# Kernel tuning notes

Hardware: AMD Instinct MI355X
Metric: run time of the kernel (lower is better)

Reference implementation:

```python
import jax, jax.numpy as jnp
import numpy as np

B, N, E = 256, 128, 262144
LABEL_DIM, MAX_DEGREE, RW_DIM = 29, 16, 16
F = 128
NUM_LABELS = LABEL_DIM + MAX_DEGREE + RW_DIM  # 61
SK_ITER, SK_TAU = 6, 1.0


def _edges(k):
    k1, k2, k3 = jax.random.split(k, 3)
    g = jax.random.randint(k1, (E,), 0, B)
    src = g * N + jax.random.randint(k2, (E,), 0, N)
    dst = g * N + jax.random.randint(k3, (E,), 0, N)
    return src, dst


def setup_inputs():
    key = jax.random.key(0)
    ks = jax.random.split(key, 20)
    ntot = B * N
    s = 0.05
    nrm = lambda k, shp: jax.random.normal(k, shp, dtype=jnp.float32) * s
    src1, dst1 = _edges(ks[3])
    src2, dst2 = _edges(ks[7])
    return {
        'x1': jax.random.uniform(ks[0], (ntot, LABEL_DIM), dtype=jnp.float32),
        'cent1': jax.random.randint(ks[1], (ntot,), 0, MAX_DEGREE),
        'rw1': jax.random.uniform(ks[2], (ntot, RW_DIM), dtype=jnp.float32),
        'src1': src1, 'dst1': dst1,
        'x2': jax.random.uniform(ks[4], (ntot, LABEL_DIM), dtype=jnp.float32),
        'cent2': jax.random.randint(ks[5], (ntot,), 0, MAX_DEGREE),
        'rw2': jax.random.uniform(ks[6], (ntot, RW_DIM), dtype=jnp.float32),
        'src2': src2, 'dst2': dst2,
        'degree_emb': nrm(ks[8], (MAX_DEGREE, MAX_DEGREE)),
        'init_W': nrm(ks[9], (NUM_LABELS, F)), 'init_b': jnp.zeros((F,), jnp.float32),
        'W1': nrm(ks[10], (F, F)), 'b1': jnp.zeros((F,), jnp.float32),
        'W2': nrm(ks[11], (F, F)), 'b2': jnp.zeros((F,), jnp.float32),
        'W3': nrm(ks[12], (F, F)), 'b3': jnp.zeros((F,), jnp.float32),
        'A_aff': nrm(ks[13], (F, F)) + jnp.eye(F, dtype=jnp.float32),
        'sc_W1': nrm(ks[14], (8 * F, 64)), 'sc_b1': jnp.zeros((64,), jnp.float32),
        'sc_W2': nrm(ks[15], (64, 1)), 'sc_b2': jnp.zeros((1,), jnp.float32),
        'topk': 8,
    }


def gcn_conv(x, W, b, src, dst):
    # GCNConv: x' = D^{-1/2} (A + I) D^{-1/2} x W + b
    n = x.shape[0]
    h = x @ W
    loops = jnp.arange(n)
    s = jnp.concatenate([src, loops])
    d = jnp.concatenate([dst, loops])
    deg = jax.ops.segment_sum(jnp.ones_like(d, dtype=h.dtype), d, n)
    dinv = jax.lax.rsqrt(jnp.maximum(deg, 1.0))
    w = dinv[s] * dinv[d]
    return jax.ops.segment_sum(h[s] * w[:, None], d, n) + b


def conv_pass(feat, src, dst, W1, b1, W2, b2, W3, b3):
    f1 = gcn_conv(feat, W1, b1, src, dst)
    f2 = gcn_conv(jax.nn.relu(f1), W2, b2, src, dst)
    f3 = gcn_conv(jax.nn.relu(f2), W3, b3, src, dst)
    return f1, f2, f3


def affinity(xa, xb, A):
    Xa = xa.reshape(B, N, -1)
    Xb = xb.reshape(B, N, -1)
    return jnp.einsum('bif,fg,bjg->bij', Xa, A, Xb)


def soft_topk(scores, ks_tgt, n_iter, tau):
    # Entropic-OT soft top-k (Xie et al.) over flattened affinity entries vs 2 anchors,
    # normalized by SK_ITER log-domain Sinkhorn iterations.
    b, n, m = scores.shape
    L = n * m
    x = scores.reshape(b, L)
    a_lo = x.min(axis=1, keepdims=True) - 1.0
    a_hi = x.max(axis=1, keepdims=True) + 1.0
    anchors = jnp.concatenate([a_lo, a_hi], axis=1)      # [b, 2]
    logK = -jnp.abs(x[:, :, None] - anchors[:, None, :]) / tau  # [b, L, 2]
    log_mu = jnp.full((b, L), -jnp.log(float(L)), dtype=x.dtype)
    k = ks_tgt[:, None]
    nu = jnp.concatenate([(L - k) / L, k / L], axis=1)   # [b, 2]
    log_nu = jnp.log(nu)

    def body(carry, _):
        f, g = carry
        f = log_mu - jax.nn.logsumexp(logK + g[:, None, :], axis=2)
        g = log_nu - jax.nn.logsumexp(logK + f[:, :, None], axis=1)
        return (f, g), None

    init = (jnp.zeros((b, L), x.dtype), jnp.zeros((b, 2), x.dtype))
    (f, g), _ = jax.lax.scan(body, init, None, length=n_iter)
    gamma = jnp.exp(logK + f[:, :, None] + g[:, None, :])
    prob = (gamma[:, :, 1] * L).reshape(b, n, m)
    return gamma, prob


def reference(x1, cent1, rw1, src1, dst1, x2, cent2, rw2, src2, dst2,
              degree_emb, init_W, init_b, W1, b1, W2, b2, W3, b3, A_aff,
              sc_W1, sc_b1, sc_W2, sc_b2, topk):
    feat1 = jax.nn.relu(jnp.concatenate([x1, degree_emb[cent1], rw1], axis=1) @ init_W + init_b)
    feat2 = jax.nn.relu(jnp.concatenate([x2, degree_emb[cent2], rw2], axis=1) @ init_W + init_b)
    f11, f12, f13 = conv_pass(feat1, src1, dst1, W1, b1, W2, b2, W3, b3)
    f21, f22, f23 = conv_pass(feat2, src2, dst2, W1, b1, W2, b2, W3, b3)

    gt_ks = jnp.full((B,), topk / 2.0, dtype=feat1.dtype)
    _, sim1 = soft_topk(affinity(feat1, feat2, A_aff), gt_ks, SK_ITER, SK_TAU)
    _, sim2 = soft_topk(affinity(f13, f23, A_aff), gt_ks, SK_ITER, SK_TAU)

    gf1 = jnp.concatenate([feat1, f11, f12, f13], axis=1).reshape(B, N, -1).sum(axis=1)   # global_add_pool
    gf2 = jnp.concatenate([feat2, f21, f22, f23], axis=1).reshape(B, N, -1).max(axis=1)   # global_max_pool
    scores = jnp.concatenate([gf1, gf2], axis=1)  # [B, 8F]
    h = jax.nn.relu(scores @ sc_W1 + sc_b1)
    ged = jax.nn.sigmoid((h @ sc_W2 + sc_b2).reshape(-1))
    return ged, sim1, sim2
```

## Files before the change

kernel.cpp:

```cpp
#include <hip/hip_runtime.h>
#include <math.h>

#define BATCH 256
#define NNODE 128
#define NT    32768
#define FDIM  128
#define NEDGE 262144
#define LBL   29
#define MAXDEG 16
#define RWD   16
#define NTF   (NT * FDIM)

__global__ void k_deg2(const int* __restrict__ dst1, const int* __restrict__ dst2,
                       int* __restrict__ d1, int* __restrict__ d2) {
  int e = blockIdx.x * 256 + threadIdx.x;
  if (e < NEDGE) atomicAdd(&d1[dst1[e]], 1);
  else if (e < 2 * NEDGE) atomicAdd(&d2[dst2[e - NEDGE]], 1);
}
__global__ __launch_bounds__(1024) void k_scan2(const int* __restrict__ degi1,
                                                int* __restrict__ ofs1, int* __restrict__ cur1,
                                                float* __restrict__ dinv1,
                                                const int* __restrict__ degi2,
                                                int* __restrict__ ofs2, int* __restrict__ cur2,
                                                float* __restrict__ dinv2) {
  const int* degi = blockIdx.x ? degi2 : degi1;
  int* ofs   = blockIdx.x ? ofs2  : ofs1;
  int* cur   = blockIdx.x ? cur2  : cur1;
  float* dnv = blockIdx.x ? dinv2 : dinv1;
  __shared__ int part[1024];
  int t = threadIdx.x;
  int base = t * 32;
  int loc[32]; int sum = 0;
#pragma unroll
  for (int u = 0; u < 32; ++u) {
    int dg = degi[base + u];
    loc[u] = sum; sum += dg;
    dnv[base + u] = rsqrtf((float)(dg + 1));
  }
  part[t] = sum;
  __syncthreads();
  for (int off = 1; off < 1024; off <<= 1) {
    int v = (t >= off) ? part[t - off] : 0;
    __syncthreads();
    part[t] += v;
    __syncthreads();
  }
  int excl = (t == 0) ? 0 : part[t - 1];
#pragma unroll
  for (int u = 0; u < 32; ++u) {
    int o = excl + loc[u];
    ofs[base + u] = o; cur[base + u] = o;
  }
}
__global__ void k_fill2(const int* __restrict__ src1, const int* __restrict__ dst1,
                        int* __restrict__ cur1, int* __restrict__ csr1,
                        const int* __restrict__ src2, const int* __restrict__ dst2,
                        int* __restrict__ cur2, int* __restrict__ csr2) {
  int e = blockIdx.x * 256 + threadIdx.x;
  if (e < NEDGE) {
    int pos = atomicAdd(&cur1[dst1[e]], 1);
    csr1[pos] = src1[e];
  } else if (e < 2 * NEDGE) {
    e -= NEDGE;
    int pos = atomicAdd(&cur2[dst2[e]], 1);
    csr2[pos] = src2[e];
  }
}

__global__ __launch_bounds__(256, 2) void k_chain(
    const float* __restrict__ x1, const int* __restrict__ cent1, const float* __restrict__ rw1,
    const float* __restrict__ x2, const int* __restrict__ cent2, const float* __restrict__ rw2,
    const float* __restrict__ demb,
    const float* __restrict__ initW, const float* __restrict__ initb,
    const float* __restrict__ W1, const float* __restrict__ b1,
    const float* __restrict__ W2, const float* __restrict__ b2,
    const float* __restrict__ W3, const float* __restrict__ b3,
    const int* __restrict__ ofs1, const int* __restrict__ end1, const int* __restrict__ csr1,
    const int* __restrict__ ofs2, const int* __restrict__ end2, const int* __restrict__ csr2,
    const float* __restrict__ dinv1, const float* __restrict__ dinv2,
    float* __restrict__ feat1G, float* __restrict__ feat2G,
    float* __restrict__ f13G, float* __restrict__ f23G,
    float* __restrict__ gfs) {
  __shared__ float X[128 * 132];
  __shared__ float WcB[16 * 132];
  __shared__ float dvL[128];
  __shared__ float bL[128];
  __shared__ int   oL[128], enL[128];

  const int t = threadIdx.x;
  const int side = blockIdx.x >> 8;
  const int g = blockIdx.x & 255;
  const int nb = g * NNODE;

  const float* xg    = side ? x2 : x1;
  const int*   centg = side ? cent2 : cent1;
  const float* rwg   = side ? rw2 : rw1;
  const int*   ofsg  = side ? ofs2 : ofs1;
  const int*   endg  = side ? end2 : end1;
  const int*   csrg  = side ? csr2 : csr1;
  const float* dinvg = side ? dinv2 : dinv1;
  float* featG = side ? feat2G : feat1G;
  float* f3G   = side ? f23G : f13G;

  const int e_base = ofsg[nb];
  if (t < 128) {
    dvL[t] = dinvg[nb + t];
    oL[t]  = ofsg[nb + t] - e_base;
    enL[t] = endg[nb + t] - e_base;
  }
  {
    int d = t >> 1, sub = t & 1;
    int node = nb + d;
    int ct = centg[node];
    const float* xr = xg + (size_t)node * LBL;
    const float* er = demb + ct * MAXDEG;
    const float* rr = rwg + (size_t)node * RWD;
    for (int c = sub * 34; c < sub * 34 + 34; ++c) {
      float v = 0.f;
      if (c < LBL) v = xr[c];
      else if (c < LBL + MAXDEG) v = er[c - LBL];
      else if (c < 61) v = rr[c - 45];
      X[d * 68 + c] = v;
    }
  }
  __syncthreads();

  const int rg = t >> 3;
  const int jq = (t & 7) * 4;

  {
    float acc[4][16] = {};
    for (int kc = 0; kc < 64; kc += 16) {
      __syncthreads();
#pragma unroll
      for (int u = 0; u < 2; ++u) {
        int ll = t + 256 * u;
        int row = ll >> 5, c4 = (ll & 31) * 4;
        int gk = kc + row;
        float4 w = (gk < 61) ? *reinterpret_cast<const float4*>(&initW[(size_t)gk * FDIM + c4])
                             : make_float4(0.f, 0.f, 0.f, 0.f);
        *reinterpret_cast<float4*>(&WcB[row * 132 + c4]) = w;
      }
      if (kc == 0 && t < 128) bL[t] = initb[t];
      __syncthreads();
      for (int kk = 0; kk < 16; kk += 4) {
        float av[4][4];
#pragma unroll
        for (int r = 0; r < 4; ++r) {
          float4 tmp = *reinterpret_cast<const float4*>(&X[(rg + 32 * r) * 68 + kc + kk]);
          av[r][0] = tmp.x; av[r][1] = tmp.y; av[r][2] = tmp.z; av[r][3] = tmp.w;
        }
#pragma unroll
        for (int c = 0; c < 4; ++c) {
          float4 w0 = *reinterpret_cast<const float4*>(&WcB[(kk + c) * 132 + jq]);
          float4 w1 = *reinterpret_cast<const float4*>(&WcB[(kk + c) * 132 + 32 + jq]);
          float4 w2 = *reinterpret_cast<const float4*>(&WcB[(kk + c) * 132 + 64 + jq]);
          float4 w3 = *reinterpret_cast<const float4*>(&WcB[(kk + c) * 132 + 96 + jq]);
#pragma unroll
          for (int r = 0; r < 4; ++r) {
            float a = av[r][c];
            acc[r][0]  += a * w0.x; acc[r][1]  += a * w0.y; acc[r][2]  += a * w0.z; acc[r][3]  += a * w0.w;
            acc[r][4]  += a * w1.x; acc[r][5]  += a * w1.y; acc[r][6]  += a * w1.z; acc[r][7]  += a * w1.w;
            acc[r][8]  += a * w2.x; acc[r][9]  += a * w2.y; acc[r][10] += a * w2.z; acc[r][11] += a * w2.w;
            acc[r][12] += a * w3.x; acc[r][13] += a * w3.y; acc[r][14] += a * w3.z; acc[r][15] += a * w3.w;
          }
        }
      }
    }
    __syncthreads();
#pragma unroll
    for (int r = 0; r < 4; ++r) {
      int row = rg + 32 * r;
#pragma unroll
      for (int q = 0; q < 4; ++q) {
        int col = q * 32 + jq;
        float4 bl = *reinterpret_cast<const float4*>(&bL[col]);
        float4 o = make_float4(fmaxf(acc[r][q * 4 + 0] + bl.x, 0.f),
                               fmaxf(acc[r][q * 4 + 1] + bl.y, 0.f),
                               fmaxf(acc[r][q * 4 + 2] + bl.z, 0.f),
                               fmaxf(acc[r][q * 4 + 3] + bl.w, 0.f));
        *reinterpret_cast<float4*>(&X[row * 132 + col]) = o;
        *reinterpret_cast<float4*>(&featG[(size_t)(nb + row) * FDIM + col]) = o;
      }
    }
    __syncthreads();
  }

#define POOL_LAYER(layer)                                                            \
  {                                                                                  \
    int j4 = (t & 31) * 4, qq = t >> 5;                                              \
    float4 pv = side ? make_float4(-INFINITY, -INFINITY, -INFINITY, -INFINITY)       \
                     : make_float4(0.f, 0.f, 0.f, 0.f);                              \
    for (int r = 0; r < 16; ++r) {                                                   \
      float4 fv = *reinterpret_cast<const float4*>(&X[(qq * 16 + r) * 132 + j4]);    \
      if (side) { pv.x = fmaxf(pv.x, fv.x); pv.y = fmaxf(pv.y, fv.y);                \
                  pv.z = fmaxf(pv.z, fv.z); pv.w = fmaxf(pv.w, fv.w); }              \
      else      { pv.x += fv.x; pv.y += fv.y; pv.z += fv.z; pv.w += fv.w; }          \
    }                                                                                \
    *reinterpret_cast<float4*>(&WcB[qq * 128 + j4]) = pv;                            \
    __syncthreads();                                                                 \
    if (t < 128) {                                                                   \
      float v = side ? -INFINITY : 0.f;                                              \
      for (int q2 = 0; q2 < 8; ++q2) {                                               \
        float w2 = WcB[q2 * 128 + t];                                                \
        v = side ? fmaxf(v, w2) : (v + w2);                                          \
      }                                                                              \
      gfs[g * 1024 + side * 512 + (layer) * 128 + t] = v;                            \
    }                                                                                \
  }

  POOL_LAYER(0)

  for (int l = 0; l < 3; ++l) {
    const float* Wg = (l == 0) ? W1 : (l == 1) ? W2 : W3;
    const float* bg = (l == 0) ? b1 : (l == 1) ? b2 : b3;
    float acc[4][16] = {};
    for (int kc = 0; kc < 128; kc += 16) {
      __syncthreads();
#pragma unroll
      for (int u = 0; u < 2; ++u) {
        int ll = t + 256 * u;
        int row = ll >> 5, c4 = (ll & 31) * 4;
        *reinterpret_cast<float4*>(&WcB[row * 132 + c4]) =
            *reinterpret_cast<const float4*>(&Wg[(size_t)(kc + row) * FDIM + c4]);
      }
      if (kc == 0 && t < 128) bL[t] = bg[t];
      __syncthreads();
      for (int kk = 0; kk < 16; kk += 4) {
        float av[4][4];
#pragma unroll
        for (int r = 0; r < 4; ++r) {
          float4 tmp = *reinterpret_cast<const float4*>(&X[(rg + 32 * r) * 132 + kc + kk]);
          if (l > 0) {
            tmp.x = fmaxf(tmp.x, 0.f); tmp.y = fmaxf(tmp.y, 0.f);
            tmp.z = fmaxf(tmp.z, 0.f); tmp.w = fmaxf(tmp.w, 0.f);
          }
          av[r][0] = tmp.x; av[r][1] = tmp.y; av[r][2] = tmp.z; av[r][3] = tmp.w;
        }
#pragma unroll
        for (int c = 0; c < 4; ++c) {
          float4 w0 = *reinterpret_cast<const float4*>(&WcB[(kk + c) * 132 + jq]);
          float4 w1 = *reinterpret_cast<const float4*>(&WcB[(kk + c) * 132 + 32 + jq]);
          float4 w2 = *reinterpret_cast<const float4*>(&WcB[(kk + c) * 132 + 64 + jq]);
          float4 w3 = *reinterpret_cast<const float4*>(&WcB[(kk + c) * 132 + 96 + jq]);
#pragma unroll
          for (int r = 0; r < 4; ++r) {
            float a = av[r][c];
            acc[r][0]  += a * w0.x; acc[r][1]  += a * w0.y; acc[r][2]  += a * w0.z; acc[r][3]  += a * w0.w;
            acc[r][4]  += a * w1.x; acc[r][5]  += a * w1.y; acc[r][6]  += a * w1.z; acc[r][7]  += a * w1.w;
            acc[r][8]  += a * w2.x; acc[r][9]  += a * w2.y; acc[r][10] += a * w2.z; acc[r][11] += a * w2.w;
            acc[r][12] += a * w3.x; acc[r][13] += a * w3.y; acc[r][14] += a * w3.z; acc[r][15] += a * w3.w;
          }
        }
      }
    }
    __syncthreads();
#pragma unroll
    for (int r = 0; r < 4; ++r) {
      int row = rg + 32 * r;
#pragma unroll
      for (int q = 0; q < 4; ++q) {
        int col = q * 32 + jq;
        *reinterpret_cast<float4*>(&X[row * 132 + col]) =
            make_float4(acc[r][q * 4 + 0], acc[r][q * 4 + 1],
                        acc[r][q * 4 + 2], acc[r][q * 4 + 3]);
      }
    }
    __syncthreads();

    {
      int d = t >> 1, fc = (t & 1) * 64;
      float dd = dvL[d];
      float4 a[16];
#pragma unroll
      for (int u = 0; u < 16; ++u) {
        float4 hv = *reinterpret_cast<const float4*>(&X[d * 132 + fc + u * 4]);
        a[u] = make_float4(dd * hv.x, dd * hv.y, dd * hv.z, dd * hv.w);
      }
      int o0 = oL[d], o1 = enL[d];
      int sj = (o0 < o1) ? (csrg[e_base + o0] - nb) : 0;
      for (int j = o0; j < o1; ++j) {
        int sn = (j + 1 < o1) ? (csrg[e_base + j + 1] - nb) : 0;
        float w = dvL[sj];
#pragma unroll
        for (int u = 0; u < 16; ++u) {
          float4 hv = *reinterpret_cast<const float4*>(&X[sj * 132 + fc + u * 4]);
          a[u].x += w * hv.x; a[u].y += w * hv.y; a[u].z += w * hv.z; a[u].w += w * hv.w;
        }
        sj = sn;
      }
      __syncthreads();
#pragma unroll
      for (int u = 0; u < 16; ++u) {
        float4 bl = *reinterpret_cast<const float4*>(&bL[fc + u * 4]);
        float4 o = make_float4(bl.x + dd * a[u].x, bl.y + dd * a[u].y,
                               bl.z + dd * a[u].z, bl.w + dd * a[u].w);
        *reinterpret_cast<float4*>(&X[d * 132 + fc + u * 4]) = o;
        if (l == 2)
          *reinterpret_cast<float4*>(&f3G[(size_t)(nb + d) * FDIM + fc + u * 4]) = o;
      }
    }
    __syncthreads();

    POOL_LAYER(l + 1)
  }
#undef POOL_LAYER
}

__global__ __launch_bounds__(1024) void k_sim(const float* __restrict__ F1s1,
                                              const float* __restrict__ F2s1,
                                              const float* __restrict__ F1s2,
                                              const float* __restrict__ F2s2,
                                              const float* __restrict__ Aaff,
                                              const int* __restrict__ topk,
                                              float* __restrict__ S1,
                                              float* __restrict__ S2) {
  __shared__ float X1[128 * 132];
  __shared__ float X2[128 * 132];
  __shared__ float WcB[16 * 132];
  __shared__ float rA[16], rB[16], bc[2];

  const int t = threadIdx.x;
  const int half = blockIdx.x >> 8;
  const int b = blockIdx.x & 255;
  const float* F1b = (half ? F1s2 : F1s1) + (size_t)b * NNODE * FDIM;
  const float* F2b = (half ? F2s2 : F2s1) + (size_t)b * NNODE * FDIM;
  float* Sout = (half ? S2 : S1) + (size_t)b * NNODE * NNODE;

#pragma unroll
  for (int p = 0; p < 4; ++p) {
    int fi = t + 1024 * p;
    int row = fi >> 5, c4 = (fi & 31) * 4;
    *reinterpret_cast<float4*>(&X1[row * 132 + c4]) =
        *reinterpret_cast<const float4*>(&F1b[(size_t)row * FDIM + c4]);
    *reinterpret_cast<float4*>(&X2[row * 132 + c4]) =
        *reinterpret_cast<const float4*>(&F2b[(size_t)row * FDIM + c4]);
  }

  const int rg = t >> 3;
  const int jq = (t & 7) * 4;

  float acc[16];
#pragma unroll
  for (int u = 0; u < 16; ++u) acc[u] = 0.f;

  for (int kc = 0; kc < 128; kc += 16) {
    __syncthreads();
    if (t < 512) {
      int row = t >> 5, c4 = (t & 31) * 4;
      *reinterpret_cast<float4*>(&WcB[row * 132 + c4]) =
          *reinterpret_cast<const float4*>(&Aaff[(size_t)(kc + row) * FDIM + c4]);
    }
    __syncthreads();
    for (int kk = 0; kk < 16; kk += 4) {
      float4 a4 = *reinterpret_cast<const float4*>(&X1[rg * 132 + kc + kk]);
      float av[4] = {a4.x, a4.y, a4.z, a4.w};
#pragma unroll
      for (int c = 0; c < 4; ++c) {
        float4 w0 = *reinterpret_cast<const float4*>(&WcB[(kk + c) * 132 + jq]);
        float4 w1 = *reinterpret_cast<const float4*>(&WcB[(kk + c) * 132 + 32 + jq]);
        float4 w2 = *reinterpret_cast<const float4*>(&WcB[(kk + c) * 132 + 64 + jq]);
        float4 w3 = *reinterpret_cast<const float4*>(&WcB[(kk + c) * 132 + 96 + jq]);
        float a = av[c];
        acc[0]  += a * w0.x; acc[1]  += a * w0.y; acc[2]  += a * w0.z; acc[3]  += a * w0.w;
        acc[4]  += a * w1.x; acc[5]  += a * w1.y; acc[6]  += a * w1.z; acc[7]  += a * w1.w;
        acc[8]  += a * w2.x; acc[9]  += a * w2.y; acc[10] += a * w2.z; acc[11] += a * w2.w;
        acc[12] += a * w3.x; acc[13] += a * w3.y; acc[14] += a * w3.z; acc[15] += a * w3.w;
      }
    }
  }
  __syncthreads();
#pragma unroll
  for (int q = 0; q < 4; ++q)
    *reinterpret_cast<float4*>(&X1[rg * 132 + 32 * q + jq]) =
        make_float4(acc[q * 4 + 0], acc[q * 4 + 1], acc[q * 4 + 2], acc[q * 4 + 3]);

#pragma unroll
  for (int u = 0; u < 16; ++u) acc[u] = 0.f;

  for (int kc = 0; kc < 128; kc += 16) {
    __syncthreads();
#pragma unroll
    for (int p = 0; p < 2; ++p) {
      int id = t + 1024 * p;
      int kkr = id >> 7, c = id & 127;
      WcB[kkr * 132 + c] = X2[c * 132 + kc + kkr];
    }
    __syncthreads();
    for (int kk = 0; kk < 16; kk += 4) {
      float4 a4 = *reinterpret_cast<const float4*>(&X1[rg * 132 + kc + kk]);
      float av[4] = {a4.x, a4.y, a4.z, a4.w};
#pragma unroll
      for (int c = 0; c < 4; ++c) {
        float4 w0 = *reinterpret_cast<const float4*>(&WcB[(kk + c) * 132 + jq]);
        float4 w1 = *reinterpret_cast<const float4*>(&WcB[(kk + c) * 132 + 32 + jq]);
        float4 w2 = *reinterpret_cast<const float4*>(&WcB[(kk + c) * 132 + 64 + jq]);
        float4 w3 = *reinterpret_cast<const float4*>(&WcB[(kk + c) * 132 + 96 + jq]);
        float a = av[c];
        acc[0]  += a * w0.x; acc[1]  += a * w0.y; acc[2]  += a * w0.z; acc[3]  += a * w0.w;
        acc[4]  += a * w1.x; acc[5]  += a * w1.y; acc[6]  += a * w1.z; acc[7]  += a * w1.w;
        acc[8]  += a * w2.x; acc[9]  += a * w2.y; acc[10] += a * w2.z; acc[11] += a * w2.w;
        acc[12] += a * w3.x; acc[13] += a * w3.y; acc[14] += a * w3.z; acc[15] += a * w3.w;
      }
    }
  }

  const int wave = t >> 6, lane = t & 63;
  {
    float mn = acc[0], mx = acc[0];
#pragma unroll
    for (int u = 1; u < 16; ++u) { mn = fminf(mn, acc[u]); mx = fmaxf(mx, acc[u]); }
    for (int off = 32; off; off >>= 1) {
      mn = fminf(mn, __shfl_down(mn, off));
      mx = fmaxf(mx, __shfl_down(mx, off));
    }
    if (lane == 0) { rA[wave] = mn; rB[wave] = mx; }
    __syncthreads();
    if (t < 16) {
      mn = rA[t]; mx = rB[t];
      for (int off = 8; off; off >>= 1) {
        mn = fminf(mn, __shfl_down(mn, off));
        mx = fmaxf(mx, __shfl_down(mx, off));
      }
      if (t == 0) { bc[0] = mn - 1.f; bc[1] = mx + 1.f; }
    }
    __syncthreads();
  }
  float a_lo = bc[0], a_hi = bc[1];

  float p[16], q[16];
#pragma unroll
  for (int u = 0; u < 16; ++u) {
    p[u] = __expf(a_lo - acc[u]);
    q[u] = __expf(acc[u] - a_hi);
  }

  const float Lf = (float)(NNODE * NNODE);
  float kt = 0.5f * (float)topk[0];

  float E0 = 1.f, E1 = 1.f, E0p = 1.f, E1p = 1.f;
  for (int it = 0; it < 6; ++it) {
    E0p = E0; E1p = E1;
    float r0 = 0.f, r1 = 0.f;
#pragma unroll
    for (int u = 0; u < 16; ++u) {
      float denom = fmaf(p[u], E0, q[u] * E1);
      float rin = __builtin_amdgcn_rcpf(denom);
      r0 = fmaf(p[u], rin, r0);
      r1 = fmaf(q[u], rin, r1);
    }
    for (int off = 32; off; off >>= 1) {
      r0 += __shfl_down(r0, off);
      r1 += __shfl_down(r1, off);
    }
    if (lane == 0) { rA[wave] = r0; rB[wave] = r1; }
    __syncthreads();
    if (t < 16) {
      r0 = rA[t]; r1 = rB[t];
      for (int off = 8; off; off >>= 1) {
        r0 += __shfl_down(r0, off);
        r1 += __shfl_down(r1, off);
      }
      if (t == 0) { bc[0] = (Lf - kt) / r0; bc[1] = kt / r1; }
    }
    __syncthreads();
    E0 = bc[0]; E1 = bc[1];
    __syncthreads();
  }

  float* xrow = Sout + (size_t)rg * NNODE;
#pragma unroll
  for (int qd = 0; qd < 4; ++qd) {
    float o[4];
#pragma unroll
    for (int j = 0; j < 4; ++j) {
      int u = qd * 4 + j;
      float denom = fmaf(p[u], E0p, q[u] * E1p);
      o[j] = q[u] * E1 * __builtin_amdgcn_rcpf(denom);
    }
    *reinterpret_cast<float4*>(&xrow[32 * qd + jq]) = make_float4(o[0], o[1], o[2], o[3]);
  }
}

__global__ __launch_bounds__(256) void k_mlp(const float* __restrict__ gfs,
                                             const float* __restrict__ W1,
                                             const float* __restrict__ b1,
                                             const float* __restrict__ W2,
                                             const float* __restrict__ b2,
                                             float* __restrict__ ged) {
  __shared__ float sm[1024];
  int b = blockIdx.x, t = threadIdx.x;
  const float* s = gfs + b * 1024;
#pragma unroll
  for (int qq = 0; qq < 4; ++qq) sm[t + 256 * qq] = s[t + 256 * qq];
  __syncthreads();
  int j4 = (t & 15) * 4, kp = t >> 4;
  float4 acc = make_float4(0.f, 0.f, 0.f, 0.f);
#pragma unroll 8
  for (int k = 0; k < 64; ++k) {
    float4 w = *reinterpret_cast<const float4*>(&W1[(size_t)(kp * 64 + k) * 64 + j4]);
    float sv = sm[kp * 64 + k];
    acc.x += sv * w.x; acc.y += sv * w.y; acc.z += sv * w.z; acc.w += sv * w.w;
  }
  __syncthreads();
  *reinterpret_cast<float4*>(&sm[kp * 64 + j4]) = acc;
  __syncthreads();
  if (t < 64) {
    float h = b1[t];
#pragma unroll
    for (int kp2 = 0; kp2 < 16; ++kp2) h += sm[kp2 * 64 + t];
    h = fmaxf(h, 0.f);
    float v = h * W2[t];
    for (int off = 32; off; off >>= 1) v += __shfl_down(v, off);
    if (t == 0) ged[b] = 1.f / (1.f + __expf(-(v + b2[0])));
  }
}

extern "C" void kernel_launch(void* const* d_in, const int* in_sizes, int n_in,
                              void* d_out, int out_size, void* d_ws, size_t ws_size,
                              hipStream_t stream) {
  (void)in_sizes; (void)n_in; (void)out_size; (void)ws_size;
  const float* x1    = (const float*)d_in[0];
  const int*   cent1 = (const int*)  d_in[1];
  const float* rw1   = (const float*)d_in[2];
  const int*   src1  = (const int*)  d_in[3];
  const int*   dst1  = (const int*)  d_in[4];
  const float* x2    = (const float*)d_in[5];
  const int*   cent2 = (const int*)  d_in[6];
  const float* rw2   = (const float*)d_in[7];
  const int*   src2  = (const int*)  d_in[8];
  const int*   dst2  = (const int*)  d_in[9];
  const float* demb  = (const float*)d_in[10];
  const float* initW = (const float*)d_in[11];
  const float* initb = (const float*)d_in[12];
  const float* W1    = (const float*)d_in[13];
  const float* b1    = (const float*)d_in[14];
  const float* W2    = (const float*)d_in[15];
  const float* b2    = (const float*)d_in[16];
  const float* W3    = (const float*)d_in[17];
  const float* b3    = (const float*)d_in[18];
  const float* Aaff  = (const float*)d_in[19];
  const float* scW1  = (const float*)d_in[20];
  const float* scb1  = (const float*)d_in[21];
  const float* scW2  = (const float*)d_in[22];
  const float* scb2  = (const float*)d_in[23];
  const int*   topk  = (const int*)  d_in[24];

  float* ws    = (float*)d_ws;
  float* feat1 = ws;
  float* feat2 = ws + (size_t)1 * NTF;
  float* f13   = ws + (size_t)2 * NTF;
  float* f23   = ws + (size_t)3 * NTF;
  float* dinv1 = ws + (size_t)4 * NTF;
  float* dinv2 = dinv1 + NT;
  float* gfs   = dinv2 + NT;

  float* ged = (float*)d_out;
  float* S1  = ged + BATCH;
  float* S2  = S1 + (size_t)BATCH * NNODE * NNODE;

  int* degi1 = (int*)S1;
  int* ofs1  = degi1 + NT;
  int* cur1  = ofs1 + NT;
  int* csr1  = cur1 + NT;
  int* degi2 = csr1 + NEDGE;
  int* ofs2  = degi2 + NT;
  int* cur2  = ofs2 + NT;
  int* csr2  = cur2 + NT;

  const int gE = NEDGE / 256;

  hipMemsetAsync(degi1, 0, NT * sizeof(int), stream);
  hipMemsetAsync(degi2, 0, NT * sizeof(int), stream);
  k_deg2<<<2 * gE, 256, 0, stream>>>(dst1, dst2, degi1, degi2);
  k_scan2<<<2, 1024, 0, stream>>>(degi1, ofs1, cur1, dinv1, degi2, ofs2, cur2, dinv2);
  k_fill2<<<2 * gE, 256, 0, stream>>>(src1, dst1, cur1, csr1, src2, dst2, cur2, csr2);

  k_chain<<<512, 256, 0, stream>>>(
      x1, cent1, rw1, x2, cent2, rw2, demb, initW, initb,
      W1, b1, W2, b2, W3, b3,
      ofs1, cur1, csr1, ofs2, cur2, csr2, dinv1, dinv2,
      feat1, feat2, f13, f23, gfs);

  k_mlp<<<BATCH, 256, 0, stream>>>(gfs, scW1, scb1, scW2, scb2, ged);

  k_sim<<<512, 1024, 0, stream>>>(feat1, feat2, f13, f23, Aaff, topk, S1, S2);
}
```

Measured before the change: 456.9 us.

## Stage full A_aff and transposed F2 in LDS once, drop per-chunk syncs

The affinity kernel now loads the whole A_aff matrix into shared memory and stores F2 transposed into shared memory at load time. The first GEMM streams each thread's F1 row straight from global memory, and the second GEMM reads the transposed F2 directly. This removes the per-16-column staging buffer and the paired barriers in each chunk of both GEMMs. In exchange, the F2 transpose writes are scalar and strided, which may cause LDS bank conflicts, and F1 reads now come uncached from global memory.

```diff
diff --git a/kernel.cpp b/kernel.cpp
--- a/kernel.cpp
+++ b/kernel.cpp
@@ -317,7 +317,6 @@
                                               float* __restrict__ S2) {
   __shared__ float X1[128 * 132];
   __shared__ float X2[128 * 132];
-  __shared__ float WcB[16 * 132];
   __shared__ float rA[16], rB[16], bc[2];
 
   const int t = threadIdx.x;
@@ -332,41 +331,46 @@
     int fi = t + 1024 * p;
     int row = fi >> 5, c4 = (fi & 31) * 4;
     *reinterpret_cast<float4*>(&X1[row * 132 + c4]) =
-        *reinterpret_cast<const float4*>(&F1b[(size_t)row * FDIM + c4]);
-    *reinterpret_cast<float4*>(&X2[row * 132 + c4]) =
-        *reinterpret_cast<const float4*>(&F2b[(size_t)row * FDIM + c4]);
-  }
+        *reinterpret_cast<const float4*>(&Aaff[(size_t)row * FDIM + c4]);
+  }
+  {
+    int row = t >> 3;
+    int cq  = (t & 7) * 4;
+#pragma unroll
+    for (int p = 0; p < 4; ++p) {
+      int c4 = p * 32 + cq;
+      float4 v = *reinterpret_cast<const float4*>(&F2b[(size_t)row * FDIM + c4]);
+      X2[(c4 + 0) * 132 + row] = v.x;
+      X2[(c4 + 1) * 132 + row] = v.y;
+      X2[(c4 + 2) * 132 + row] = v.z;
+      X2[(c4 + 3) * 132 + row] = v.w;
+    }
+  }
+  __syncthreads();
 
   const int rg = t >> 3;
   const int jq = (t & 7) * 4;
+  const float* f1row = F1b + (size_t)rg * FDIM;
 
   float acc[16];
 #pragma unroll
   for (int u = 0; u < 16; ++u) acc[u] = 0.f;
 
-  for (int kc = 0; kc < 128; kc += 16) {
-    __syncthreads();
-    if (t < 512) {
-      int row = t >> 5, c4 = (t & 31) * 4;
-      *reinterpret_cast<float4*>(&WcB[row * 132 + c4]) =
-          *reinterpret_cast<const float4*>(&Aaff[(size_t)(kc + row) * FDIM + c4]);
-    }
-    __syncthreads();
-    for (int kk = 0; kk < 16; kk += 4) {
-      float4 a4 = *reinterpret_cast<const float4*>(&X1[rg * 132 + kc + kk]);
-      float av[4] = {a4.x, a4.y, a4.z, a4.w};
-#pragma unroll
-      for (int c = 0; c < 4; ++c) {
-        float4 w0 = *reinterpret_cast<const float4*>(&WcB[(kk + c) * 132 + jq]);
-        float4 w1 = *reinterpret_cast<const float4*>(&WcB[(kk + c) * 132 + 32 + jq]);
-        float4 w2 = *reinterpret_cast<const float4*>(&WcB[(kk + c) * 132 + 64 + jq]);
-        float4 w3 = *reinterpret_cast<const float4*>(&WcB[(kk + c) * 132 + 96 + jq]);
-        float a = av[c];
-        acc[0]  += a * w0.x; acc[1]  += a * w0.y; acc[2]  += a * w0.z; acc[3]  += a * w0.w;
-        acc[4]  += a * w1.x; acc[5]  += a * w1.y; acc[6]  += a * w1.z; acc[7]  += a * w1.w;
-        acc[8]  += a * w2.x; acc[9]  += a * w2.y; acc[10] += a * w2.z; acc[11] += a * w2.w;
-        acc[12] += a * w3.x; acc[13] += a * w3.y; acc[14] += a * w3.z; acc[15] += a * w3.w;
-      }
+  for (int k0 = 0; k0 < 128; k0 += 4) {
+    float4 a4 = *reinterpret_cast<const float4*>(&f1row[k0]);
+    float av[4] = {a4.x, a4.y, a4.z, a4.w};
+#pragma unroll
+    for (int c = 0; c < 4; ++c) {
+      const float* wb = &X1[(k0 + c) * 132];
+      float4 w0 = *reinterpret_cast<const float4*>(&wb[jq]);
+      float4 w1 = *reinterpret_cast<const float4*>(&wb[32 + jq]);
+      float4 w2 = *reinterpret_cast<const float4*>(&wb[64 + jq]);
+      float4 w3 = *reinterpret_cast<const float4*>(&wb[96 + jq]);
+      float a = av[c];
+      acc[0]  += a * w0.x; acc[1]  += a * w0.y; acc[2]  += a * w0.z; acc[3]  += a * w0.w;
+      acc[4]  += a * w1.x; acc[5]  += a * w1.y; acc[6]  += a * w1.z; acc[7]  += a * w1.w;
+      acc[8]  += a * w2.x; acc[9]  += a * w2.y; acc[10] += a * w2.z; acc[11] += a * w2.w;
+      acc[12] += a * w3.x; acc[13] += a * w3.y; acc[14] += a * w3.z; acc[15] += a * w3.w;
     }
   }
   __syncthreads();
@@ -377,31 +381,23 @@
 
 #pragma unroll
   for (int u = 0; u < 16; ++u) acc[u] = 0.f;
-
-  for (int kc = 0; kc < 128; kc += 16) {
-    __syncthreads();
-#pragma unroll
-    for (int p = 0; p < 2; ++p) {
-      int id = t + 1024 * p;
-      int kkr = id >> 7, c = id & 127;
-      WcB[kkr * 132 + c] = X2[c * 132 + kc + kkr];
-    }
-    __syncthreads();
-    for (int kk = 0; kk < 16; kk += 4) {
-      float4 a4 = *reinterpret_cast<const float4*>(&X1[rg * 132 + kc + kk]);
-      float av[4] = {a4.x, a4.y, a4.z, a4.w};
-#pragma unroll
-      for (int c = 0; c < 4; ++c) {
-        float4 w0 = *reinterpret_cast<const float4*>(&WcB[(kk + c) * 132 + jq]);
-        float4 w1 = *reinterpret_cast<const float4*>(&WcB[(kk + c) * 132 + 32 + jq]);
-        float4 w2 = *reinterpret_cast<const float4*>(&WcB[(kk + c) * 132 + 64 + jq]);
-        float4 w3 = *reinterpret_cast<const float4*>(&WcB[(kk + c) * 132 + 96 + jq]);
-        float a = av[c];
-        acc[0]  += a * w0.x; acc[1]  += a * w0.y; acc[2]  += a * w0.z; acc[3]  += a * w0.w;
-        acc[4]  += a * w1.x; acc[5]  += a * w1.y; acc[6]  += a * w1.z; acc[7]  += a * w1.w;
-        acc[8]  += a * w2.x; acc[9]  += a * w2.y; acc[10] += a * w2.z; acc[11] += a * w2.w;
-        acc[12] += a * w3.x; acc[13] += a * w3.y; acc[14] += a * w3.z; acc[15] += a * w3.w;
-      }
+  __syncthreads();
+
+  for (int k0 = 0; k0 < 128; k0 += 4) {
+    float4 a4 = *reinterpret_cast<const float4*>(&X1[rg * 132 + k0]);
+    float av[4] = {a4.x, a4.y, a4.z, a4.w};
+#pragma unroll
+    for (int c = 0; c < 4; ++c) {
+      const float* wb = &X2[(k0 + c) * 132];
+      float4 w0 = *reinterpret_cast<const float4*>(&wb[jq]);
+      float4 w1 = *reinterpret_cast<const float4*>(&wb[32 + jq]);
+      float4 w2 = *reinterpret_cast<const float4*>(&wb[64 + jq]);
+      float4 w3 = *reinterpret_cast<const float4*>(&wb[96 + jq]);
+      float a = av[c];
+      acc[0]  += a * w0.x; acc[1]  += a * w0.y; acc[2]  += a * w0.z; acc[3]  += a * w0.w;
+      acc[4]  += a * w1.x; acc[5]  += a * w1.y; acc[6]  += a * w1.z; acc[7]  += a * w1.w;
+      acc[8]  += a * w2.x; acc[9]  += a * w2.y; acc[10] += a * w2.z; acc[11] += a * w2.w;
+      acc[12] += a * w3.x; acc[13] += a * w3.y; acc[14] += a * w3.z; acc[15] += a * w3.w;
     }
   }
 
```

Result: faster. 442.8 us (-3.1%).
